# Optimization experiments

Measured on AMD Instinct MI355X. Metric: run time of the kernel, lower is better.

Reference implementation:

```python
import jax, jax.numpy as jnp
import numpy as np


def hardsigmoid(x):
    # relu6(x + 3) / 6
    return jnp.clip(x + 3.0, 0.0, 6.0) / 6.0


def setup_inputs() -> dict:
    key = jax.random.key(0)
    k1, k2 = jax.random.split(key)
    x = jax.random.normal(k1, (16, 256, 128, 128), dtype=jnp.float32)
    # Conv2d(2, 1, kernel_size=3, bias=False): weight [out=1, in=2, 3, 3]
    fan_in = 2 * 3 * 3
    bound = 1.0 / np.sqrt(fan_in)
    conv_w = jax.random.uniform(k2, (1, 2, 3, 3), minval=-bound, maxval=bound, dtype=jnp.float32)
    return {"x": x, "conv_w": conv_w}


def reference(x, conv_w):
    # x: [B, C, H, W]
    avg_out = jnp.mean(x, axis=1, keepdims=True)   # [B,1,H,W]
    max_out = jnp.max(x, axis=1, keepdims=True)    # [B,1,H,W]
    y = jnp.concatenate([avg_out, max_out], axis=1)  # [B,2,H,W]
    y = jax.lax.conv_general_dilated(
        y, conv_w,
        window_strides=(1, 1),
        padding=((1, 1), (1, 1)),
        dimension_numbers=("NCHW", "OIHW", "NCHW"),
    )  # [B,1,H,W]
    y = hardsigmoid(y)
    return x * y
```

## Files before the change

### kernel.cpp

```cpp
#include <hip/hip_runtime.h>
#include <math.h>

#define BB 16
#define CC 256
#define HH 128
#define WW 128
#define HWP (HH * WW)
#define P4  (HWP / 4)
#define PLANE ((size_t)CC * HWP)

typedef float f4 __attribute__((ext_vector_type(4)));

__global__ __launch_bounds__(256) void reduce_kernel(
    const float* __restrict__ x,
    float* __restrict__ psum,
    float* __restrict__ pmax)
{
    int t    = blockIdx.x * 256 + threadIdx.x;
    int p4   = t & (P4 - 1);
    int half = (t >> 12) & 1;
    int b    = t >> 13;

    const f4* xp = (const f4*)(x + (size_t)b * PLANE + (size_t)half * 128 * HWP) + p4;

    f4 s = {0.f, 0.f, 0.f, 0.f};
    f4 m = {-INFINITY, -INFINITY, -INFINITY, -INFINITY};
    #pragma unroll 8
    for (int c = 0; c < 128; ++c) {
        f4 v = xp[c * P4];
        s.x += v.x; s.y += v.y; s.z += v.z; s.w += v.w;
        m.x = fmaxf(m.x, v.x); m.y = fmaxf(m.y, v.y);
        m.z = fmaxf(m.z, v.z); m.w = fmaxf(m.w, v.w);
    }

    f4* sp = (f4*)(psum + ((size_t)half * BB + b) * HWP) + p4;
    f4* mp = (f4*)(pmax + ((size_t)half * BB + b) * HWP) + p4;
    *sp = s;
    *mp = m;
}

__global__ __launch_bounds__(256) void conv_kernel(
    const float* __restrict__ cw,
    const float* __restrict__ psum,
    const float* __restrict__ pmax,
    float* __restrict__ amap)
{
    int t  = blockIdx.x * 256 + threadIdx.x;
    int hw = t & (HWP - 1);
    int b  = t >> 14;
    int h  = hw >> 7;
    int w  = hw & (WW - 1);

    float wa[9], wm[9];
    #pragma unroll
    for (int i = 0; i < 9; ++i) { wa[i] = cw[i]; wm[i] = cw[9 + i]; }

    const float* s0 = psum + (size_t)b * HWP;
    const float* s1 = psum + ((size_t)BB + b) * HWP;
    const float* m0 = pmax + (size_t)b * HWP;
    const float* m1 = pmax + ((size_t)BB + b) * HWP;

    float acc = 0.f;
    #pragma unroll
    for (int ki = 0; ki < 3; ++ki) {
        int hh = h + ki - 1;
        if (hh < 0 || hh >= HH) continue;
        #pragma unroll
        for (int kj = 0; kj < 3; ++kj) {
            int ww = w + kj - 1;
            if (ww < 0 || ww >= WW) continue;
            int n = hh * WW + ww;
            float avg = (s0[n] + s1[n]) * (1.f / 256.f);
            float mx  = fmaxf(m0[n], m1[n]);
            acc += wa[ki * 3 + kj] * avg + wm[ki * 3 + kj] * mx;
        }
    }
    amap[t] = fminf(fmaxf(acc + 3.f, 0.f), 6.f) * (1.f / 6.f);
}

__global__ __launch_bounds__(256) void apply_kernel(
    const float* __restrict__ x,
    const float* __restrict__ amap,
    float* __restrict__ out)
{
    int t  = blockIdx.x * 256 + threadIdx.x;
    int p4 = t & (P4 - 1);
    int g  = (t >> 12) & 3;
    int b  = t >> 14;

    f4 a = *((const f4*)(amap + (size_t)b * HWP) + p4);

    const f4* xp = (const f4*)(x   + (size_t)b * PLANE + (size_t)g * 64 * HWP) + p4;
    f4*       op = (f4*)      (out + (size_t)b * PLANE + (size_t)g * 64 * HWP) + p4;

    #pragma unroll 8
    for (int ci = 63; ci >= 0; --ci) {
        f4 v = __builtin_nontemporal_load(xp + ci * P4);
        f4 r;
        r.x = v.x * a.x; r.y = v.y * a.y; r.z = v.z * a.z; r.w = v.w * a.w;
        __builtin_nontemporal_store(r, op + ci * P4);
    }
}

extern "C" void kernel_launch(void* const* d_in, const int* in_sizes, int n_in,
                              void* d_out, int out_size, void* d_ws, size_t ws_size,
                              hipStream_t stream)
{
    const float* x  = (const float*)d_in[0];
    const float* cw = (const float*)d_in[1];
    float* out      = (float*)d_out;

    float* psum = (float*)d_ws;
    float* pmax = psum + (size_t)2 * BB * HWP;
    float* amap = pmax + (size_t)2 * BB * HWP;

    reduce_kernel<<<512,  256, 0, stream>>>(x, psum, pmax);
    conv_kernel  <<<1024, 256, 0, stream>>>(cw, psum, pmax, amap);
    apply_kernel <<<1024, 256, 0, stream>>>(x, amap, out);
}
```

Baseline: 497.4 us.

## Fuse reduce, conv and apply into one cooperative kernel with grid syncs

```diff
diff --git a/kernel.cpp b/kernel.cpp
--- a/kernel.cpp
+++ b/kernel.cpp
@@ -1,5 +1,8 @@
 #include <hip/hip_runtime.h>
+#include <hip/hip_cooperative_groups.h>
 #include <math.h>
+
+namespace cg = cooperative_groups;
 
 #define BB 16
 #define CC 256
@@ -11,6 +14,89 @@
 
 typedef float f4 __attribute__((ext_vector_type(4)));
 
+__global__ __launch_bounds__(256, 4) void fused_kernel(
+    const float* __restrict__ x,
+    const float* __restrict__ cw,
+    float* __restrict__ psum,
+    float* __restrict__ pmax,
+    float* __restrict__ amap,
+    float* __restrict__ out)
+{
+    cg::grid_group grid = cg::this_grid();
+
+    int t  = blockIdx.x * 256 + threadIdx.x;
+    int p4 = t & (P4 - 1);
+    int q  = (t >> 12) & 3;
+    int b  = t >> 14;
+
+    {
+        const f4* xp = (const f4*)(x + (size_t)b * PLANE + (size_t)q * 64 * HWP) + p4;
+        f4 s = {0.f, 0.f, 0.f, 0.f};
+        f4 m = {-INFINITY, -INFINITY, -INFINITY, -INFINITY};
+        #pragma unroll 8
+        for (int c = 0; c < 64; ++c) {
+            f4 v = xp[(size_t)c * P4];
+            s.x += v.x; s.y += v.y; s.z += v.z; s.w += v.w;
+            m.x = fmaxf(m.x, v.x); m.y = fmaxf(m.y, v.y);
+            m.z = fmaxf(m.z, v.z); m.w = fmaxf(m.w, v.w);
+        }
+        ((f4*)(psum + ((size_t)q * BB + b) * HWP))[p4] = s;
+        ((f4*)(pmax + ((size_t)q * BB + b) * HWP))[p4] = m;
+    }
+
+    grid.sync();
+
+    {
+        int hw = t & (HWP - 1);
+        int bc = t >> 14;
+        int h  = hw >> 7;
+        int w  = hw & (WW - 1);
+
+        float wa[9], wm[9];
+        #pragma unroll
+        for (int i = 0; i < 9; ++i) { wa[i] = cw[i]; wm[i] = cw[9 + i]; }
+
+        const float* s0 = psum + (size_t)bc * HWP;
+        const float* m0 = pmax + (size_t)bc * HWP;
+        const size_t qs = (size_t)BB * HWP;
+
+        float acc = 0.f;
+        #pragma unroll
+        for (int ki = 0; ki < 3; ++ki) {
+            int hh = h + ki - 1;
+            if (hh < 0 || hh >= HH) continue;
+            #pragma unroll
+            for (int kj = 0; kj < 3; ++kj) {
+                int ww = w + kj - 1;
+                if (ww < 0 || ww >= WW) continue;
+                int n = hh * WW + ww;
+                float sv = s0[n] + s0[n + qs] + s0[n + 2 * qs] + s0[n + 3 * qs];
+                float mv = fmaxf(fmaxf(m0[n], m0[n + qs]),
+                                 fmaxf(m0[n + 2 * qs], m0[n + 3 * qs]));
+                acc += wa[ki * 3 + kj] * (sv * (1.f / 256.f)) + wm[ki * 3 + kj] * mv;
+            }
+        }
+        amap[t] = fminf(fmaxf(acc + 3.f, 0.f), 6.f) * (1.f / 6.f);
+    }
+
+    grid.sync();
+
+    {
+        f4 a = *((const f4*)(amap + (size_t)b * HWP) + p4);
+
+        const f4* xp = (const f4*)(x   + (size_t)b * PLANE + (size_t)q * 64 * HWP) + p4;
+        f4*       op = (f4*)      (out + (size_t)b * PLANE + (size_t)q * 64 * HWP) + p4;
+
+        #pragma unroll 8
+        for (int ci = 63; ci >= 0; --ci) {
+            f4 v = xp[(size_t)ci * P4];
+            f4 r;
+            r.x = v.x * a.x; r.y = v.y * a.y; r.z = v.z * a.z; r.w = v.w * a.w;
+            __builtin_nontemporal_store(r, op + (size_t)ci * P4);
+        }
+    }
+}
+
 __global__ __launch_bounds__(256) void reduce_kernel(
     const float* __restrict__ x,
     float* __restrict__ psum,
@@ -27,16 +113,14 @@
     f4 m = {-INFINITY, -INFINITY, -INFINITY, -INFINITY};
     #pragma unroll 8
     for (int c = 0; c < 128; ++c) {
-        f4 v = xp[c * P4];
+        f4 v = xp[(size_t)c * P4];
         s.x += v.x; s.y += v.y; s.z += v.z; s.w += v.w;
         m.x = fmaxf(m.x, v.x); m.y = fmaxf(m.y, v.y);
         m.z = fmaxf(m.z, v.z); m.w = fmaxf(m.w, v.w);
     }
 
-    f4* sp = (f4*)(psum + ((size_t)half * BB + b) * HWP) + p4;
-    f4* mp = (f4*)(pmax + ((size_t)half * BB + b) * HWP) + p4;
-    *sp = s;
-    *mp = m;
+    ((f4*)(psum + ((size_t)half * BB + b) * HWP))[p4] = s;
+    ((f4*)(pmax + ((size_t)half * BB + b) * HWP))[p4] = m;
 }
 
 __global__ __launch_bounds__(256) void conv_kernel(
@@ -95,10 +179,10 @@
 
     #pragma unroll 8
     for (int ci = 63; ci >= 0; --ci) {
-        f4 v = __builtin_nontemporal_load(xp + ci * P4);
+        f4 v = xp[(size_t)ci * P4];
         f4 r;
         r.x = v.x * a.x; r.y = v.y * a.y; r.z = v.z * a.z; r.w = v.w * a.w;
-        __builtin_nontemporal_store(r, op + ci * P4);
+        __builtin_nontemporal_store(r, op + (size_t)ci * P4);
     }
 }
 
@@ -111,8 +195,20 @@
     float* out      = (float*)d_out;
 
     float* psum = (float*)d_ws;
-    float* pmax = psum + (size_t)2 * BB * HWP;
-    float* amap = pmax + (size_t)2 * BB * HWP;
+    float* pmax = psum + (size_t)4 * BB * HWP;
+    float* amap = pmax + (size_t)4 * BB * HWP;
+
+    int maxb = 0;
+    hipError_t qerr = hipOccupancyMaxActiveBlocksPerMultiprocessor(
+        &maxb, fused_kernel, 256, 0);
+
+    if (qerr == hipSuccess && maxb >= 4) {
+        void* args[] = { (void*)&x, (void*)&cw, (void*)&psum,
+                         (void*)&pmax, (void*)&amap, (void*)&out };
+        hipError_t lerr = hipLaunchCooperativeKernel(
+            (const void*)fused_kernel, dim3(1024), dim3(256), args, 0, stream);
+        if (lerr == hipSuccess) return;
+    }
 
     reduce_kernel<<<512,  256, 0, stream>>>(x, psum, pmax);
     conv_kernel  <<<1024, 256, 0, stream>>>(cw, psum, pmax, amap);
```

After: 728.8 us. 1.47x slower.
